# Kernel optimization log

Hardware: AMD Instinct MI355X
Metric: run time of the kernel (lower is better)

## Reference

```python
import jax, jax.numpy as jnp
import numpy as np

D_MODEL = 1024
NUM_HEADS = 16
D_K = D_MODEL // NUM_HEADS
NEG = -10000.0


def setup_inputs() -> dict:
    key = jax.random.key(0)
    ks = jax.random.split(key, 8)
    B, S = 2, 2048
    query = jax.random.normal(ks[0], (B, S, D_MODEL), dtype=jnp.float32)
    key_t = jax.random.normal(ks[1], (B, S, D_MODEL), dtype=jnp.float32)
    value = jax.random.normal(ks[2], (B, S, D_MODEL), dtype=jnp.float32)
    mask = jax.random.randint(ks[3], (B, S), 0, 2, dtype=jnp.int32)
    scale = 1.0 / np.sqrt(D_MODEL)
    Wq = jax.random.normal(ks[4], (D_MODEL, D_MODEL), dtype=jnp.float32) * scale
    Wk = jax.random.normal(ks[5], (D_MODEL, D_MODEL), dtype=jnp.float32) * scale
    Wv = jax.random.normal(ks[6], (D_MODEL, D_MODEL), dtype=jnp.float32) * scale
    Wo = jax.random.normal(ks[7], (D_MODEL, D_MODEL), dtype=jnp.float32) * scale
    return {"query": query, "key": key_t, "value": value, "mask": mask,
            "Wq": Wq, "Wk": Wk, "Wv": Wv, "Wo": Wo}


def reference(query, key, value, mask, Wq, Wk, Wv, Wo):
    B, Sq, _ = query.shape
    Sk = key.shape[1]
    # Linear projections (torch Linear: x @ W.T), split heads -> [B,H,S,d_k]
    def proj(x, W, S):
        return (x @ W.T).reshape(B, S, NUM_HEADS, D_K).transpose(0, 2, 1, 3)
    Q = proj(query, Wq, Sq)
    K = proj(key, Wk, Sk)
    V = proj(value, Wv, Sk)
    # scores [B,H,Sq,Sk]
    scores = jnp.einsum("bhqd,bhkd->bhqk", Q, K) / jnp.sqrt(jnp.float32(D_K))
    # padding mask [B,Sk] -> [B,1,1,Sk]
    pad = mask[:, None, None, :]
    scores = jnp.where(pad == 0, NEG, scores)
    # causal mask (mask_future=True)
    causal = jnp.tril(jnp.ones((Sq, Sk), dtype=bool))
    scores = jnp.where(causal, scores, NEG)
    probs = jax.nn.softmax(scores, axis=-1)  # dropout p=0.0 -> identity
    out = jnp.einsum("bhqk,bhkd->bhqd", probs, V)
    out = out.transpose(0, 2, 1, 3).reshape(B, Sq, D_MODEL)
    return out @ Wo.T
```

## Files before the change

### kernel.cpp

```cpp
#include <hip/hip_runtime.h>
#include <hip/hip_bf16.h>
#include <math.h>

typedef __attribute__((ext_vector_type(8))) short s16x8;
typedef __attribute__((ext_vector_type(4))) float f32x4;

#define MFMA16(a,b,c) __builtin_amdgcn_mfma_f32_16x16x32_bf16((a),(b),(c),0,0,0)

#define GLD16(gp, lp) __builtin_amdgcn_global_load_lds( \
  (const __attribute__((address_space(1))) unsigned int*)(gp), \
  (__attribute__((address_space(3))) unsigned int*)(lp), 16, 0, 0)

static __device__ __forceinline__ unsigned short f2bu(float f) {
  __hip_bfloat16 h = __float2bfloat16(f);
  unsigned short u; __builtin_memcpy(&u, &h, 2); return u;
}
static __device__ __forceinline__ float b2f(unsigned short u) {
  unsigned int x = ((unsigned int)u) << 16; float f; __builtin_memcpy(&f, &x, 4); return f;
}

__global__ __launch_bounds__(256) void cast_all(const float* __restrict__ q, const float* __restrict__ k,
                                                const float* __restrict__ v,
                                                const float* __restrict__ Wq, const float* __restrict__ Wk,
                                                const float* __restrict__ Wv, const float* __restrict__ Wo,
                                                unsigned short* __restrict__ qc, unsigned short* __restrict__ kc,
                                                unsigned short* __restrict__ vc,
                                                unsigned short* __restrict__ wq, unsigned short* __restrict__ wk,
                                                unsigned short* __restrict__ wv, unsigned short* __restrict__ wo) {
  const int y = blockIdx.y;
  const float* in; unsigned short* out; int n4;
  switch (y) {
    case 0: in = q;  out = qc; n4 = 1048576; break;
    case 1: in = k;  out = kc; n4 = 1048576; break;
    case 2: in = v;  out = vc; n4 = 1048576; break;
    case 3: in = Wq; out = wq; n4 = 262144; break;
    case 4: in = Wk; out = wk; n4 = 262144; break;
    case 5: in = Wv; out = wv; n4 = 262144; break;
    default: in = Wo; out = wo; n4 = 262144; break;
  }
  int i = blockIdx.x * 256 + threadIdx.x;
  if (i < n4) {
    float4 val = *(const float4*)(in + (size_t)i * 4);
    unsigned int p0 = (unsigned int)f2bu(val.x) | ((unsigned int)f2bu(val.y) << 16);
    unsigned int p1 = (unsigned int)f2bu(val.z) | ((unsigned int)f2bu(val.w) << 16);
    uint2 pk; pk.x = p0; pk.y = p1;
    *(uint2*)(out + (size_t)i * 4) = pk;
  }
}

static __device__ __forceinline__ void gemm_core(const unsigned short* __restrict__ Aw,
                                                 const unsigned short* __restrict__ Bw,
                                                 int m0, int n0,
                                                 f32x4 (&acc)[4][4],
                                                 unsigned short (*As)[64], unsigned short (*Bs)[64]) {
  const int K = 1024;
  const int tid = threadIdx.x;
  const int lane = tid & 63, wave = tid >> 6;
  const int wm = wave >> 1, wn = wave & 1;
  const int row16 = lane & 15, kgrp = lane >> 4;
  const int srow = lane >> 3, sslot = (lane & 7) ^ srow;
  const int sw = row16 & 7;

  for (int k0 = 0; k0 < K; k0 += 64) {
#pragma unroll
    for (int i = 0; i < 4; i++) {
      int rr = (wave * 4 + i) * 8 + srow;
      GLD16(Aw + (size_t)(m0 + rr) * K + k0 + sslot * 8, (char*)As + (wave * 4 + i) * 1024);
      GLD16(Bw + (size_t)(n0 + rr) * K + k0 + sslot * 8, (char*)Bs + (wave * 4 + i) * 1024);
    }
    __syncthreads();

#pragma unroll
    for (int kk = 0; kk < 2; kk++) {
      s16x8 af[4], bfr[4];
#pragma unroll
      for (int mi = 0; mi < 4; mi++) {
        int rr = wm * 64 + mi * 16 + row16;
        af[mi] = *(const s16x8*)((char*)&As[rr][0] + ((kk * 4 + kgrp) ^ sw) * 16);
      }
#pragma unroll
      for (int ni = 0; ni < 4; ni++) {
        int rr = wn * 64 + ni * 16 + row16;
        bfr[ni] = *(const s16x8*)((char*)&Bs[rr][0] + ((kk * 4 + kgrp) ^ sw) * 16);
      }
#pragma unroll
      for (int mi = 0; mi < 4; mi++)
#pragma unroll
        for (int ni = 0; ni < 4; ni++)
          acc[mi][ni] = MFMA16(af[mi], bfr[ni], acc[mi][ni]);
    }
    __syncthreads();
  }
}

__global__ __launch_bounds__(256) void qkv_gemm(const unsigned short* __restrict__ qc,
                                                const unsigned short* __restrict__ kc,
                                                const unsigned short* __restrict__ vc,
                                                const unsigned short* __restrict__ Wqb,
                                                const unsigned short* __restrict__ Wkb,
                                                const unsigned short* __restrict__ Wvb,
                                                unsigned short* __restrict__ Qb,
                                                unsigned short* __restrict__ Kb,
                                                unsigned short* __restrict__ Vt) {
  __shared__ unsigned short As[128][64];
  __shared__ unsigned short Bs[128][64];
  const int xcd = blockIdx.x & 7, u = blockIdx.x >> 3;
  const int g = xcd * 12 + (u >> 3);
  const int z = g >> 5, mstrip = g & 31;
  const int m0 = mstrip * 128, n0 = (u & 7) * 128;

  const unsigned short* A = (z == 0) ? qc : (z == 1) ? kc : vc;
  const unsigned short* Bw = (z == 0) ? Wqb : (z == 1) ? Wkb : Wvb;

  f32x4 acc[4][4] = {};
  gemm_core(A, Bw, m0, n0, acc, As, Bs);

  const int lane = threadIdx.x & 63, wave = threadIdx.x >> 6;
  const int wm = wave >> 1, wn = wave & 1;
  const int row16 = lane & 15, kgrp = lane >> 4;

  if (z < 2) {
    unsigned short* C = z ? Kb : Qb;
#pragma unroll
    for (int mi = 0; mi < 4; mi++)
#pragma unroll
      for (int ni = 0; ni < 4; ni++)
#pragma unroll
        for (int r = 0; r < 4; r++) {
          int row = m0 + wm * 64 + mi * 16 + kgrp * 4 + r;
          int col = n0 + wn * 64 + ni * 16 + row16;
          C[(size_t)row * 1024 + col] = f2bu(acc[mi][ni][r]);
        }
  } else {
#pragma unroll
    for (int mi = 0; mi < 4; mi++)
#pragma unroll
      for (int ni = 0; ni < 4; ni++) {
        int mb = m0 + wm * 64 + mi * 16 + kgrp * 4;
        int col = n0 + wn * 64 + ni * 16 + row16;
        int bb = mb >> 11, s = mb & 2047;
        unsigned int p0 = (unsigned int)f2bu(acc[mi][ni][0]) | ((unsigned int)f2bu(acc[mi][ni][1]) << 16);
        unsigned int p1 = (unsigned int)f2bu(acc[mi][ni][2]) | ((unsigned int)f2bu(acc[mi][ni][3]) << 16);
        uint2 pk; pk.x = p0; pk.y = p1;
        *(uint2*)&Vt[(((size_t)(bb * 1024 + col)) << 11) + s] = pk;
      }
  }
}

__global__ __launch_bounds__(256) void gemm_wo(const unsigned short* __restrict__ A,
                                               const unsigned short* __restrict__ Bw,
                                               float* __restrict__ C) {
  __shared__ unsigned short As[128][64];
  __shared__ unsigned short Bs[128][64];
  const int xcd = blockIdx.x & 7, u = blockIdx.x >> 3;
  const int g = xcd * 4 + (u >> 3);
  const int m0 = g * 128, n0 = (u & 7) * 128;

  f32x4 acc[4][4] = {};
  gemm_core(A, Bw, m0, n0, acc, As, Bs);

  const int lane = threadIdx.x & 63, wave = threadIdx.x >> 6;
  const int wm = wave >> 1, wn = wave & 1;
  const int row16 = lane & 15, kgrp = lane >> 4;
#pragma unroll
  for (int mi = 0; mi < 4; mi++)
#pragma unroll
    for (int ni = 0; ni < 4; ni++)
#pragma unroll
      for (int r = 0; r < 4; r++) {
        int row = m0 + wm * 64 + mi * 16 + kgrp * 4 + r;
        int col = n0 + wn * 64 + ni * 16 + row16;
        C[(size_t)row * 1024 + col] = acc[mi][ni][r];
      }
}

__global__ __launch_bounds__(256) void fu_pen_kernel(const int* __restrict__ mask, int* __restrict__ fu,
                                                     float* __restrict__ pen) {
  const int S = 2048;
  int b = blockIdx.x;
  __shared__ int red[256];
  int best = S;
  for (int k = threadIdx.x; k < S; k += 256) {
    int mv = mask[b * S + k];
    pen[b * S + k] = mv ? 0.0f : -30000.0f;
    if (mv != 0 && k < best) best = k;
  }
  red[threadIdx.x] = best;
  __syncthreads();
  for (int s = 128; s > 0; s >>= 1) {
    if (threadIdx.x < s) red[threadIdx.x] = min(red[threadIdx.x], red[threadIdx.x + s]);
    __syncthreads();
  }
  if (threadIdx.x == 0) fu[b] = red[0];
}

__global__ __launch_bounds__(256) void reduce_vt(const unsigned short* __restrict__ Vt,
                                                 float* __restrict__ vsum) {
  __shared__ float red[256];
  const unsigned short* p = Vt + ((size_t)blockIdx.x << 11) + threadIdx.x * 8;
  uint4 u = *(const uint4*)p;
  float s = b2f((unsigned short)(u.x & 0xffff));
  s += b2f((unsigned short)(u.x >> 16));
  s += b2f((unsigned short)(u.y & 0xffff));
  s += b2f((unsigned short)(u.y >> 16));
  s += b2f((unsigned short)(u.z & 0xffff));
  s += b2f((unsigned short)(u.z >> 16));
  s += b2f((unsigned short)(u.w & 0xffff));
  s += b2f((unsigned short)(u.w >> 16));
  red[threadIdx.x] = s;
  __syncthreads();
  for (int st = 128; st > 0; st >>= 1) {
    if (threadIdx.x < st) red[threadIdx.x] += red[threadIdx.x + st];
    __syncthreads();
  }
  if (threadIdx.x == 0) vsum[blockIdx.x] = red[0];
}

__global__ __launch_bounds__(256) void flash_attn6(const unsigned short* __restrict__ Q,
                                                   const unsigned short* __restrict__ Kp,
                                                   const unsigned short* __restrict__ Vt,
                                                   const float* __restrict__ pen,
                                                   const int* __restrict__ fu,
                                                   const float* __restrict__ vsum,
                                                   unsigned short* __restrict__ O) {
  const int S = 2048, DM = 1024;
  const float SCALE2 = 0.125f * 1.4426950408889634f;
  const int bid = blockIdx.x;
  const int qt = 31 - (bid >> 5);
  const int bh = bid & 31;
  const int b = bh >> 4, h = bh & 15;
  const int tid = threadIdx.x, lane = tid & 63, wave = tid >> 6;
  const int row16 = lane & 15, kgrp = lane >> 4;

  __shared__ unsigned short Ks[2][64][64];
  __shared__ unsigned short Vs[2][64][64];
  __shared__ unsigned short Ps[4][16][64];

  const size_t base = ((size_t)b * S) * DM + h * 64;
  const size_t vtb = ((size_t)(b * 1024 + h * 64)) * S;
  const float* penb = pen + b * S;

  const int srow = lane >> 3;
  const int sslot = (lane & 7) ^ srow;
  const int sw = row16 & 7;

  const int q0 = qt * 64 + wave * 16;
  const int qg = q0 + row16;
  const int nt = qt + 1;

  s16x8 qf0 = *(const s16x8*)&Q[base + (size_t)qg * DM + kgrp * 8];
  s16x8 qf1 = *(const s16x8*)&Q[base + (size_t)qg * DM + 32 + kgrp * 8];

  const short ONE = 0x3F80;
  const s16x8 ones8 = {ONE, ONE, ONE, ONE, ONE, ONE, ONE, ONE};

  f32x4 oacc[4] = {};
  f32x4 lacc = {};
  float m_run = -1e30f;

  auto stage = [&](int t, int bf) {
    const int kb = t * 64;
#pragma unroll
    for (int c2 = 0; c2 < 2; c2++) {
      const int r = wave * 16 + c2 * 8 + srow;
      GLD16(Kp + base + (size_t)(kb + r) * DM + sslot * 8,
            (char*)&Ks[bf][0][0] + (wave * 2 + c2) * 1024);
      GLD16(Vt + vtb + (size_t)r * S + kb + sslot * 8,
            (char*)&Vs[bf][0][0] + (wave * 2 + c2) * 1024);
    }
  };

  stage(0, 0);
  asm volatile("s_waitcnt vmcnt(0)" ::: "memory");
  __syncthreads();

  int cur = 0;
  for (int t = 0; t < nt; ++t) {
    if (t + 1 < nt) stage(t + 1, cur ^ 1);
    const int kb = t * 64;

    float4 pv[4];
#pragma unroll
    for (int nf = 0; nf < 4; nf++)
      pv[nf] = *(const float4*)&penb[kb + nf * 16 + kgrp * 4];

    f32x4 sc[4];
    __builtin_amdgcn_s_setprio(1);
#pragma unroll
    for (int nf = 0; nf < 4; nf++) {
      const int rr = nf * 16 + row16;
      s16x8 k0 = *(const s16x8*)&Ks[cur][rr][(kgrp ^ sw) * 8];
      s16x8 k1 = *(const s16x8*)&Ks[cur][rr][((4 + kgrp) ^ sw) * 8];
      f32x4 a = {};
      a = MFMA16(k0, qf0, a);
      a = MFMA16(k1, qf1, a);
      sc[nf] = a;
    }
    __builtin_amdgcn_s_setprio(0);

#pragma unroll
    for (int nf = 0; nf < 4; nf++) {
      sc[nf][0] = fmaf(sc[nf][0], SCALE2, pv[nf].x);
      sc[nf][1] = fmaf(sc[nf][1], SCALE2, pv[nf].y);
      sc[nf][2] = fmaf(sc[nf][2], SCALE2, pv[nf].z);
      sc[nf][3] = fmaf(sc[nf][3], SCALE2, pv[nf].w);
    }
    if (t == nt - 1) {
#pragma unroll
      for (int nf = 0; nf < 4; nf++) {
        const int kbase = kb + nf * 16 + kgrp * 4;
#pragma unroll
        for (int r = 0; r < 4; r++)
          if (kbase + r > qg) sc[nf][r] = -30000.0f;
      }
    }

    float t01 = fmaxf(fmaxf(sc[0][0], sc[0][1]), fmaxf(sc[0][2], sc[0][3]));
    float t23 = fmaxf(fmaxf(sc[1][0], sc[1][1]), fmaxf(sc[1][2], sc[1][3]));
    float t45 = fmaxf(fmaxf(sc[2][0], sc[2][1]), fmaxf(sc[2][2], sc[2][3]));
    float t67 = fmaxf(fmaxf(sc[3][0], sc[3][1]), fmaxf(sc[3][2], sc[3][3]));
    float tmax = fmaxf(fmaxf(t01, t23), fmaxf(t45, t67));
    tmax = fmaxf(tmax, __shfl_xor(tmax, 16));
    tmax = fmaxf(tmax, __shfl_xor(tmax, 32));

    if (__any(tmax > m_run)) {
      float mnew = fmaxf(m_run, tmax);
      float alpha = __builtin_exp2f(m_run - mnew);
      m_run = mnew;
      lacc[0] *= alpha; lacc[1] *= alpha; lacc[2] *= alpha; lacc[3] *= alpha;
#pragma unroll
      for (int nf2 = 0; nf2 < 4; nf2++)
#pragma unroll
        for (int r = 0; r < 4; r++) oacc[nf2][r] *= alpha;
    }

#pragma unroll
    for (int nf = 0; nf < 4; nf++)
#pragma unroll
      for (int r = 0; r < 4; r++)
        sc[nf][r] = __builtin_exp2f(sc[nf][r] - m_run);

#pragma unroll
    for (int nf = 0; nf < 4; nf++) {
      uint2 pk;
      pk.x = (unsigned int)f2bu(sc[nf][0]) | ((unsigned int)f2bu(sc[nf][1]) << 16);
      pk.y = (unsigned int)f2bu(sc[nf][2]) | ((unsigned int)f2bu(sc[nf][3]) << 16);
      const int slot = (nf * 2 + (kgrp >> 1)) ^ sw;
      *(uint2*)((char*)&Ps[wave][row16][0] + slot * 16 + (kgrp & 1) * 8) = pk;
    }
    s16x8 pf0 = *(const s16x8*)((char*)&Ps[wave][row16][0] + (kgrp ^ sw) * 16);
    s16x8 pf1 = *(const s16x8*)((char*)&Ps[wave][row16][0] + ((4 + kgrp) ^ sw) * 16);

    __builtin_amdgcn_s_setprio(1);
    lacc = MFMA16(ones8, pf0, lacc);
    lacc = MFMA16(ones8, pf1, lacc);
#pragma unroll
    for (int nf2 = 0; nf2 < 4; nf2++) {
      const int rr = nf2 * 16 + row16;
      s16x8 v0 = *(const s16x8*)&Vs[cur][rr][(kgrp ^ sw) * 8];
      s16x8 v1 = *(const s16x8*)&Vs[cur][rr][((4 + kgrp) ^ sw) * 8];
      oacc[nf2] = MFMA16(v0, pf0, oacc[nf2]);
      oacc[nf2] = MFMA16(v1, pf1, oacc[nf2]);
    }
    __builtin_amdgcn_s_setprio(0);

    asm volatile("s_waitcnt vmcnt(0)" ::: "memory");
    __syncthreads();
    cur ^= 1;
  }

  const int fub = fu[b];
  const float* vs = vsum + b * DM + h * 64;
  const float rl = 1.0f / lacc[0];
#pragma unroll
  for (int nf2 = 0; nf2 < 4; nf2++) {
    const int d0 = nf2 * 16 + kgrp * 4;
    float v0 = oacc[nf2][0] * rl, v1 = oacc[nf2][1] * rl;
    float v2 = oacc[nf2][2] * rl, v3 = oacc[nf2][3] * rl;
    if (qg < fub) {
      float4 vv = *(const float4*)&vs[d0];
      v0 = vv.x * (1.0f / 2048.0f);
      v1 = vv.y * (1.0f / 2048.0f);
      v2 = vv.z * (1.0f / 2048.0f);
      v3 = vv.w * (1.0f / 2048.0f);
    }
    uint2 pk;
    pk.x = (unsigned int)f2bu(v0) | ((unsigned int)f2bu(v1) << 16);
    pk.y = (unsigned int)f2bu(v2) | ((unsigned int)f2bu(v3) << 16);
    *(uint2*)&O[base + (size_t)qg * DM + d0] = pk;
  }
}

extern "C" void kernel_launch(void* const* d_in, const int* in_sizes, int n_in,
                              void* d_out, int out_size, void* d_ws, size_t ws_size,
                              hipStream_t stream) {
  const float* q    = (const float*)d_in[0];
  const float* k    = (const float*)d_in[1];
  const float* v    = (const float*)d_in[2];
  const int*   mask = (const int*)d_in[3];
  const float* Wq   = (const float*)d_in[4];
  const float* Wk   = (const float*)d_in[5];
  const float* Wv   = (const float*)d_in[6];
  const float* Wo   = (const float*)d_in[7];
  float* out = (float*)d_out;
  char* ws = (char*)d_ws;

  unsigned short* Wqb  = (unsigned short*)(ws + (size_t)0);
  unsigned short* Wkb  = (unsigned short*)(ws + ((size_t)2 << 20));
  unsigned short* Wvb  = (unsigned short*)(ws + ((size_t)4 << 20));
  unsigned short* Wob  = (unsigned short*)(ws + ((size_t)6 << 20));
  unsigned short* vc   = (unsigned short*)(ws + ((size_t)8 << 20));
  unsigned short* attn = (unsigned short*)(ws + ((size_t)8 << 20));
  unsigned short* Qb   = (unsigned short*)(ws + ((size_t)16 << 20));
  unsigned short* Kb   = (unsigned short*)(ws + ((size_t)24 << 20));
  unsigned short* Vt   = (unsigned short*)(ws + ((size_t)32 << 20));
  float* vsum          = (float*)(ws + ((size_t)40 << 20));
  int*   fub           = (int*)(ws + ((size_t)40 << 20) + (64 << 10));
  float* pen           = (float*)(ws + ((size_t)40 << 20) + (68 << 10));
  unsigned short* qc   = (unsigned short*)d_out;
  unsigned short* kc   = (unsigned short*)d_out + 4194304;

  cast_all<<<dim3(4096, 7), 256, 0, stream>>>(q, k, v, Wq, Wk, Wv, Wo,
                                              qc, kc, vc, Wqb, Wkb, Wvb, Wob);

  qkv_gemm<<<768, 256, 0, stream>>>(qc, kc, vc, Wqb, Wkb, Wvb, Qb, Kb, Vt);

  fu_pen_kernel<<<2, 256, 0, stream>>>(mask, fub, pen);
  reduce_vt<<<2048, 256, 0, stream>>>(Vt, vsum);

  flash_attn6<<<1024, 256, 0, stream>>>(Qb, Kb, Vt, pen, fub, vsum, attn);

  gemm_wo<<<256, 256, 0, stream>>>(attn, Wob, out);
}
```

Measured before the change: 143.3 us.

## Double flash-attention KV tile to 128 and fold mask prep into cast kernel

The attention kernel now processes 128 keys per iteration instead of 64. This halves the number of loop iterations and their barrier/wait overheads, and reduces the per-tile max shuffles by deferring the cross-lane reduction into the rescale branch. K, V and P shared-memory buffers double in size (about 80KB per block), which may reduce blocks per CU. For even query tiles the last iteration also does up to 64 columns of masked, wasted work. Separately, the mask/penalty kernel is merged into the cast kernel as an extra grid row to remove one launch, though that row launches thousands of blocks that exit immediately.

```diff
diff --git a/kernel.cpp b/kernel.cpp
--- a/kernel.cpp
+++ b/kernel.cpp
@@ -23,11 +23,33 @@
                                                 const float* __restrict__ v,
                                                 const float* __restrict__ Wq, const float* __restrict__ Wk,
                                                 const float* __restrict__ Wv, const float* __restrict__ Wo,
+                                                const int* __restrict__ mask,
                                                 unsigned short* __restrict__ qc, unsigned short* __restrict__ kc,
                                                 unsigned short* __restrict__ vc,
                                                 unsigned short* __restrict__ wq, unsigned short* __restrict__ wk,
-                                                unsigned short* __restrict__ wv, unsigned short* __restrict__ wo) {
+                                                unsigned short* __restrict__ wv, unsigned short* __restrict__ wo,
+                                                int* __restrict__ fu, float* __restrict__ pen) {
   const int y = blockIdx.y;
+  if (y == 7) {
+    if (blockIdx.x >= 2) return;
+    const int S = 2048;
+    int b = blockIdx.x;
+    __shared__ int red[256];
+    int best = S;
+    for (int kk = threadIdx.x; kk < S; kk += 256) {
+      int mv = mask[b * S + kk];
+      pen[b * S + kk] = mv ? 0.0f : -30000.0f;
+      if (mv != 0 && kk < best) best = kk;
+    }
+    red[threadIdx.x] = best;
+    __syncthreads();
+    for (int s = 128; s > 0; s >>= 1) {
+      if (threadIdx.x < s) red[threadIdx.x] = min(red[threadIdx.x], red[threadIdx.x + s]);
+      __syncthreads();
+    }
+    if (threadIdx.x == 0) fu[b] = red[0];
+    return;
+  }
   const float* in; unsigned short* out; int n4;
   switch (y) {
     case 0: in = q;  out = qc; n4 = 1048576; break;
@@ -172,26 +194,6 @@
         int col = n0 + wn * 64 + ni * 16 + row16;
         C[(size_t)row * 1024 + col] = acc[mi][ni][r];
       }
-}
-
-__global__ __launch_bounds__(256) void fu_pen_kernel(const int* __restrict__ mask, int* __restrict__ fu,
-                                                     float* __restrict__ pen) {
-  const int S = 2048;
-  int b = blockIdx.x;
-  __shared__ int red[256];
-  int best = S;
-  for (int k = threadIdx.x; k < S; k += 256) {
-    int mv = mask[b * S + k];
-    pen[b * S + k] = mv ? 0.0f : -30000.0f;
-    if (mv != 0 && k < best) best = k;
-  }
-  red[threadIdx.x] = best;
-  __syncthreads();
-  for (int s = 128; s > 0; s >>= 1) {
-    if (threadIdx.x < s) red[threadIdx.x] = min(red[threadIdx.x], red[threadIdx.x + s]);
-    __syncthreads();
-  }
-  if (threadIdx.x == 0) fu[b] = red[0];
 }
 
 __global__ __launch_bounds__(256) void reduce_vt(const unsigned short* __restrict__ Vt,
@@ -216,7 +218,7 @@
   if (threadIdx.x == 0) vsum[blockIdx.x] = red[0];
 }
 
-__global__ __launch_bounds__(256) void flash_attn6(const unsigned short* __restrict__ Q,
+__global__ __launch_bounds__(256) void flash_attn7(const unsigned short* __restrict__ Q,
                                                    const unsigned short* __restrict__ Kp,
                                                    const unsigned short* __restrict__ Vt,
                                                    const float* __restrict__ pen,
@@ -232,21 +234,21 @@
   const int tid = threadIdx.x, lane = tid & 63, wave = tid >> 6;
   const int row16 = lane & 15, kgrp = lane >> 4;
 
-  __shared__ unsigned short Ks[2][64][64];
-  __shared__ unsigned short Vs[2][64][64];
-  __shared__ unsigned short Ps[4][16][64];
+  __shared__ unsigned short Ks[2][128][64];
+  __shared__ unsigned short Vs[2][64][128];
+  __shared__ unsigned short Ps[4][16][128];
 
   const size_t base = ((size_t)b * S) * DM + h * 64;
   const size_t vtb = ((size_t)(b * 1024 + h * 64)) * S;
   const float* penb = pen + b * S;
 
-  const int srow = lane >> 3;
-  const int sslot = (lane & 7) ^ srow;
+  const int srowK = lane >> 3;
+  const int sslotK = (lane & 7) ^ srowK;
   const int sw = row16 & 7;
 
   const int q0 = qt * 64 + wave * 16;
   const int qg = q0 + row16;
-  const int nt = qt + 1;
+  const int nt = (qt + 2) >> 1;
 
   s16x8 qf0 = *(const s16x8*)&Q[base + (size_t)qg * DM + kgrp * 8];
   s16x8 qf1 = *(const s16x8*)&Q[base + (size_t)qg * DM + 32 + kgrp * 8];
@@ -259,14 +261,19 @@
   float m_run = -1e30f;
 
   auto stage = [&](int t, int bf) {
-    const int kb = t * 64;
-#pragma unroll
-    for (int c2 = 0; c2 < 2; c2++) {
-      const int r = wave * 16 + c2 * 8 + srow;
-      GLD16(Kp + base + (size_t)(kb + r) * DM + sslot * 8,
-            (char*)&Ks[bf][0][0] + (wave * 2 + c2) * 1024);
-      GLD16(Vt + vtb + (size_t)r * S + kb + sslot * 8,
-            (char*)&Vs[bf][0][0] + (wave * 2 + c2) * 1024);
+    const int kb = t * 128;
+#pragma unroll
+    for (int c = 0; c < 4; c++) {
+      const int r = wave * 32 + c * 8 + srowK;
+      GLD16(Kp + base + (size_t)(kb + r) * DM + sslotK * 8,
+            (char*)&Ks[bf][0][0] + (wave * 4 + c) * 1024);
+    }
+#pragma unroll
+    for (int c = 0; c < 4; c++) {
+      const int r = wave * 16 + c * 4 + (lane >> 4);
+      const int sl = (lane & 15) ^ (r & 7);
+      GLD16(Vt + vtb + (size_t)r * S + kb + sl * 8,
+            (char*)&Vs[bf][0][0] + (wave * 4 + c) * 1024);
     }
   };
 
@@ -277,20 +284,20 @@
   int cur = 0;
   for (int t = 0; t < nt; ++t) {
     if (t + 1 < nt) stage(t + 1, cur ^ 1);
-    const int kb = t * 64;
-
-    float4 pv[4];
-#pragma unroll
-    for (int nf = 0; nf < 4; nf++)
+    const int kb = t * 128;
+
+    float4 pv[8];
+#pragma unroll
+    for (int nf = 0; nf < 8; nf++)
       pv[nf] = *(const float4*)&penb[kb + nf * 16 + kgrp * 4];
 
-    f32x4 sc[4];
+    f32x4 sc[8];
     __builtin_amdgcn_s_setprio(1);
 #pragma unroll
-    for (int nf = 0; nf < 4; nf++) {
+    for (int nf = 0; nf < 8; nf++) {
       const int rr = nf * 16 + row16;
-      s16x8 k0 = *(const s16x8*)&Ks[cur][rr][(kgrp ^ sw) * 8];
-      s16x8 k1 = *(const s16x8*)&Ks[cur][rr][((4 + kgrp) ^ sw) * 8];
+      s16x8 k0 = *(const s16x8*)((char*)&Ks[cur][rr][0] + ((0 + kgrp) ^ sw) * 16);
+      s16x8 k1 = *(const s16x8*)((char*)&Ks[cur][rr][0] + ((4 + kgrp) ^ sw) * 16);
       f32x4 a = {};
       a = MFMA16(k0, qf0, a);
       a = MFMA16(k1, qf1, a);
@@ -299,7 +306,7 @@
     __builtin_amdgcn_s_setprio(0);
 
 #pragma unroll
-    for (int nf = 0; nf < 4; nf++) {
+    for (int nf = 0; nf < 8; nf++) {
       sc[nf][0] = fmaf(sc[nf][0], SCALE2, pv[nf].x);
       sc[nf][1] = fmaf(sc[nf][1], SCALE2, pv[nf].y);
       sc[nf][2] = fmaf(sc[nf][2], SCALE2, pv[nf].z);
@@ -307,7 +314,7 @@
     }
     if (t == nt - 1) {
 #pragma unroll
-      for (int nf = 0; nf < 4; nf++) {
+      for (int nf = 0; nf < 8; nf++) {
         const int kbase = kb + nf * 16 + kgrp * 4;
 #pragma unroll
         for (int r = 0; r < 4; r++)
@@ -315,16 +322,15 @@
       }
     }
 
-    float t01 = fmaxf(fmaxf(sc[0][0], sc[0][1]), fmaxf(sc[0][2], sc[0][3]));
-    float t23 = fmaxf(fmaxf(sc[1][0], sc[1][1]), fmaxf(sc[1][2], sc[1][3]));
-    float t45 = fmaxf(fmaxf(sc[2][0], sc[2][1]), fmaxf(sc[2][2], sc[2][3]));
-    float t67 = fmaxf(fmaxf(sc[3][0], sc[3][1]), fmaxf(sc[3][2], sc[3][3]));
-    float tmax = fmaxf(fmaxf(t01, t23), fmaxf(t45, t67));
-    tmax = fmaxf(tmax, __shfl_xor(tmax, 16));
-    tmax = fmaxf(tmax, __shfl_xor(tmax, 32));
+    float tmax = fmaxf(fmaxf(sc[0][0], sc[0][1]), fmaxf(sc[0][2], sc[0][3]));
+#pragma unroll
+    for (int nf = 1; nf < 8; nf++)
+      tmax = fmaxf(tmax, fmaxf(fmaxf(sc[nf][0], sc[nf][1]), fmaxf(sc[nf][2], sc[nf][3])));
 
     if (__any(tmax > m_run)) {
-      float mnew = fmaxf(m_run, tmax);
+      float wmax = fmaxf(tmax, __shfl_xor(tmax, 16));
+      wmax = fmaxf(wmax, __shfl_xor(wmax, 32));
+      float mnew = fmaxf(m_run, wmax);
       float alpha = __builtin_exp2f(m_run - mnew);
       m_run = mnew;
       lacc[0] *= alpha; lacc[1] *= alpha; lacc[2] *= alpha; lacc[3] *= alpha;
@@ -335,32 +341,35 @@
     }
 
 #pragma unroll
-    for (int nf = 0; nf < 4; nf++)
+    for (int nf = 0; nf < 8; nf++)
 #pragma unroll
       for (int r = 0; r < 4; r++)
         sc[nf][r] = __builtin_exp2f(sc[nf][r] - m_run);
 
 #pragma unroll
-    for (int nf = 0; nf < 4; nf++) {
+    for (int nf = 0; nf < 8; nf++) {
       uint2 pk;
       pk.x = (unsigned int)f2bu(sc[nf][0]) | ((unsigned int)f2bu(sc[nf][1]) << 16);
       pk.y = (unsigned int)f2bu(sc[nf][2]) | ((unsigned int)f2bu(sc[nf][3]) << 16);
       const int slot = (nf * 2 + (kgrp >> 1)) ^ sw;
       *(uint2*)((char*)&Ps[wave][row16][0] + slot * 16 + (kgrp & 1) * 8) = pk;
     }
-    s16x8 pf0 = *(const s16x8*)((char*)&Ps[wave][row16][0] + (kgrp ^ sw) * 16);
-    s16x8 pf1 = *(const s16x8*)((char*)&Ps[wave][row16][0] + ((4 + kgrp) ^ sw) * 16);
+    s16x8 pf[4];
+#pragma unroll
+    for (int kk = 0; kk < 4; kk++)
+      pf[kk] = *(const s16x8*)((char*)&Ps[wave][row16][0] + ((kk * 4 + kgrp) ^ sw) * 16);
 
     __builtin_amdgcn_s_setprio(1);
-    lacc = MFMA16(ones8, pf0, lacc);
-    lacc = MFMA16(ones8, pf1, lacc);
+#pragma unroll
+    for (int kk = 0; kk < 4; kk++) lacc = MFMA16(ones8, pf[kk], lacc);
 #pragma unroll
     for (int nf2 = 0; nf2 < 4; nf2++) {
       const int rr = nf2 * 16 + row16;
-      s16x8 v0 = *(const s16x8*)&Vs[cur][rr][(kgrp ^ sw) * 8];
-      s16x8 v1 = *(const s16x8*)&Vs[cur][rr][((4 + kgrp) ^ sw) * 8];
-      oacc[nf2] = MFMA16(v0, pf0, oacc[nf2]);
-      oacc[nf2] = MFMA16(v1, pf1, oacc[nf2]);
+#pragma unroll
+      for (int kk = 0; kk < 4; kk++) {
+        s16x8 vv = *(const s16x8*)((char*)&Vs[cur][rr][0] + ((kk * 4 + kgrp) ^ sw) * 16);
+        oacc[nf2] = MFMA16(vv, pf[kk], oacc[nf2]);
+      }
     }
     __builtin_amdgcn_s_setprio(0);
 
@@ -420,15 +429,14 @@
   unsigned short* qc   = (unsigned short*)d_out;
   unsigned short* kc   = (unsigned short*)d_out + 4194304;
 
-  cast_all<<<dim3(4096, 7), 256, 0, stream>>>(q, k, v, Wq, Wk, Wv, Wo,
-                                              qc, kc, vc, Wqb, Wkb, Wvb, Wob);
+  cast_all<<<dim3(4096, 8), 256, 0, stream>>>(q, k, v, Wq, Wk, Wv, Wo, mask,
+                                              qc, kc, vc, Wqb, Wkb, Wvb, Wob, fub, pen);
 
   qkv_gemm<<<768, 256, 0, stream>>>(qc, kc, vc, Wqb, Wkb, Wvb, Qb, Kb, Vt);
 
-  fu_pen_kernel<<<2, 256, 0, stream>>>(mask, fub, pen);
   reduce_vt<<<2048, 256, 0, stream>>>(Vt, vsum);
 
-  flash_attn6<<<1024, 256, 0, stream>>>(Qb, Kb, Vt, pen, fub, vsum, attn);
+  flash_attn7<<<1024, 256, 0, stream>>>(Qb, Kb, Vt, pen, fub, vsum, attn);
 
   gemm_wo<<<256, 256, 0, stream>>>(attn, Wob, out);
 }
```

After: 145.5 us. No clear change (+1.5%).

## Fold softmax scale into Wq, replace additive pad penalty with bitmask, merge mask prep

Applied to the files above, without the earlier changes.

Pre-scales Wq by the softmax scale times log2(e) during the bf16 cast, so the attention kernel no longer applies an FMA per score. The padding penalty becomes a 16-bit-per-key AND mask applied to the packed bf16 probabilities, and the mask/first-unmasked computation moves into cast_all as an extra grid row, removing one launch. The cross-lane max shuffle now runs only when some lane's local max rises, and bf16 packing uses the hardware v_cvt_pk_bf16_f32 instruction. Masked keys now take part in the running max, which shifts the numerics slightly, and the per-lane max tracking could differ from the old row max semantics.

```diff
diff --git a/kernel.cpp b/kernel.cpp
--- a/kernel.cpp
+++ b/kernel.cpp
@@ -17,23 +17,52 @@
 }
 static __device__ __forceinline__ float b2f(unsigned short u) {
   unsigned int x = ((unsigned int)u) << 16; float f; __builtin_memcpy(&f, &x, 4); return f;
+}
+static __device__ __forceinline__ unsigned int cvtpk(float lo, float hi) {
+  unsigned int r;
+  asm("v_cvt_pk_bf16_f32 %0, %1, %2" : "=v"(r) : "v"(lo), "v"(hi));
+  return r;
 }
 
 __global__ __launch_bounds__(256) void cast_all(const float* __restrict__ q, const float* __restrict__ k,
                                                 const float* __restrict__ v,
                                                 const float* __restrict__ Wq, const float* __restrict__ Wk,
                                                 const float* __restrict__ Wv, const float* __restrict__ Wo,
+                                                const int* __restrict__ mask,
                                                 unsigned short* __restrict__ qc, unsigned short* __restrict__ kc,
                                                 unsigned short* __restrict__ vc,
                                                 unsigned short* __restrict__ wq, unsigned short* __restrict__ wk,
-                                                unsigned short* __restrict__ wv, unsigned short* __restrict__ wo) {
+                                                unsigned short* __restrict__ wv, unsigned short* __restrict__ wo,
+                                                int* __restrict__ fu, unsigned int* __restrict__ pm) {
+  const float SCALE2 = 0.125f * 1.4426950408889634f;
   const int y = blockIdx.y;
-  const float* in; unsigned short* out; int n4;
+  if (y == 7) {
+    if (blockIdx.x >= 2) return;
+    const int S = 2048;
+    int b = blockIdx.x;
+    __shared__ int red[256];
+    int best = S;
+    for (int kk = threadIdx.x; kk < 1024; kk += 256) {
+      int m0 = mask[b * S + 2 * kk], m1 = mask[b * S + 2 * kk + 1];
+      pm[b * 1024 + kk] = (m0 ? 0xFFFFu : 0u) | (m1 ? 0xFFFF0000u : 0u);
+      if (m1) best = min(best, 2 * kk + 1);
+      if (m0) best = min(best, 2 * kk);
+    }
+    red[threadIdx.x] = best;
+    __syncthreads();
+    for (int s = 128; s > 0; s >>= 1) {
+      if (threadIdx.x < s) red[threadIdx.x] = min(red[threadIdx.x], red[threadIdx.x + s]);
+      __syncthreads();
+    }
+    if (threadIdx.x == 0) fu[b] = red[0];
+    return;
+  }
+  const float* in; unsigned short* out; int n4; float scl = 1.0f;
   switch (y) {
     case 0: in = q;  out = qc; n4 = 1048576; break;
     case 1: in = k;  out = kc; n4 = 1048576; break;
     case 2: in = v;  out = vc; n4 = 1048576; break;
-    case 3: in = Wq; out = wq; n4 = 262144; break;
+    case 3: in = Wq; out = wq; n4 = 262144; scl = SCALE2; break;
     case 4: in = Wk; out = wk; n4 = 262144; break;
     case 5: in = Wv; out = wv; n4 = 262144; break;
     default: in = Wo; out = wo; n4 = 262144; break;
@@ -41,9 +70,9 @@
   int i = blockIdx.x * 256 + threadIdx.x;
   if (i < n4) {
     float4 val = *(const float4*)(in + (size_t)i * 4);
-    unsigned int p0 = (unsigned int)f2bu(val.x) | ((unsigned int)f2bu(val.y) << 16);
-    unsigned int p1 = (unsigned int)f2bu(val.z) | ((unsigned int)f2bu(val.w) << 16);
-    uint2 pk; pk.x = p0; pk.y = p1;
+    uint2 pk;
+    pk.x = cvtpk(val.x * scl, val.y * scl);
+    pk.y = cvtpk(val.z * scl, val.w * scl);
     *(uint2*)(out + (size_t)i * 4) = pk;
   }
 }
@@ -139,9 +168,9 @@
         int mb = m0 + wm * 64 + mi * 16 + kgrp * 4;
         int col = n0 + wn * 64 + ni * 16 + row16;
         int bb = mb >> 11, s = mb & 2047;
-        unsigned int p0 = (unsigned int)f2bu(acc[mi][ni][0]) | ((unsigned int)f2bu(acc[mi][ni][1]) << 16);
-        unsigned int p1 = (unsigned int)f2bu(acc[mi][ni][2]) | ((unsigned int)f2bu(acc[mi][ni][3]) << 16);
-        uint2 pk; pk.x = p0; pk.y = p1;
+        uint2 pk;
+        pk.x = cvtpk(acc[mi][ni][0], acc[mi][ni][1]);
+        pk.y = cvtpk(acc[mi][ni][2], acc[mi][ni][3]);
         *(uint2*)&Vt[(((size_t)(bb * 1024 + col)) << 11) + s] = pk;
       }
   }
@@ -172,26 +201,6 @@
         int col = n0 + wn * 64 + ni * 16 + row16;
         C[(size_t)row * 1024 + col] = acc[mi][ni][r];
       }
-}
-
-__global__ __launch_bounds__(256) void fu_pen_kernel(const int* __restrict__ mask, int* __restrict__ fu,
-                                                     float* __restrict__ pen) {
-  const int S = 2048;
-  int b = blockIdx.x;
-  __shared__ int red[256];
-  int best = S;
-  for (int k = threadIdx.x; k < S; k += 256) {
-    int mv = mask[b * S + k];
-    pen[b * S + k] = mv ? 0.0f : -30000.0f;
-    if (mv != 0 && k < best) best = k;
-  }
-  red[threadIdx.x] = best;
-  __syncthreads();
-  for (int s = 128; s > 0; s >>= 1) {
-    if (threadIdx.x < s) red[threadIdx.x] = min(red[threadIdx.x], red[threadIdx.x + s]);
-    __syncthreads();
-  }
-  if (threadIdx.x == 0) fu[b] = red[0];
 }
 
 __global__ __launch_bounds__(256) void reduce_vt(const unsigned short* __restrict__ Vt,
@@ -216,15 +225,14 @@
   if (threadIdx.x == 0) vsum[blockIdx.x] = red[0];
 }
 
-__global__ __launch_bounds__(256) void flash_attn6(const unsigned short* __restrict__ Q,
+__global__ __launch_bounds__(256) void flash_attn8(const unsigned short* __restrict__ Q,
                                                    const unsigned short* __restrict__ Kp,
                                                    const unsigned short* __restrict__ Vt,
-                                                   const float* __restrict__ pen,
+                                                   const unsigned int* __restrict__ pm,
                                                    const int* __restrict__ fu,
                                                    const float* __restrict__ vsum,
                                                    unsigned short* __restrict__ O) {
   const int S = 2048, DM = 1024;
-  const float SCALE2 = 0.125f * 1.4426950408889634f;
   const int bid = blockIdx.x;
   const int qt = 31 - (bid >> 5);
   const int bh = bid & 31;
@@ -238,7 +246,7 @@
 
   const size_t base = ((size_t)b * S) * DM + h * 64;
   const size_t vtb = ((size_t)(b * 1024 + h * 64)) * S;
-  const float* penb = pen + b * S;
+  const unsigned int* pmb = pm + b * 1024;
 
   const int srow = lane >> 3;
   const int sslot = (lane & 7) ^ srow;
@@ -279,10 +287,10 @@
     if (t + 1 < nt) stage(t + 1, cur ^ 1);
     const int kb = t * 64;
 
-    float4 pv[4];
+    uint2 pmv[4];
 #pragma unroll
     for (int nf = 0; nf < 4; nf++)
-      pv[nf] = *(const float4*)&penb[kb + nf * 16 + kgrp * 4];
+      pmv[nf] = *(const uint2*)&pmb[(kb + nf * 16 + kgrp * 4) >> 1];
 
     f32x4 sc[4];
     __builtin_amdgcn_s_setprio(1);
@@ -298,13 +306,6 @@
     }
     __builtin_amdgcn_s_setprio(0);
 
-#pragma unroll
-    for (int nf = 0; nf < 4; nf++) {
-      sc[nf][0] = fmaf(sc[nf][0], SCALE2, pv[nf].x);
-      sc[nf][1] = fmaf(sc[nf][1], SCALE2, pv[nf].y);
-      sc[nf][2] = fmaf(sc[nf][2], SCALE2, pv[nf].z);
-      sc[nf][3] = fmaf(sc[nf][3], SCALE2, pv[nf].w);
-    }
     if (t == nt - 1) {
 #pragma unroll
       for (int nf = 0; nf < 4; nf++) {
@@ -315,18 +316,20 @@
       }
     }
 
-    float t01 = fmaxf(fmaxf(sc[0][0], sc[0][1]), fmaxf(sc[0][2], sc[0][3]));
-    float t23 = fmaxf(fmaxf(sc[1][0], sc[1][1]), fmaxf(sc[1][2], sc[1][3]));
-    float t45 = fmaxf(fmaxf(sc[2][0], sc[2][1]), fmaxf(sc[2][2], sc[2][3]));
-    float t67 = fmaxf(fmaxf(sc[3][0], sc[3][1]), fmaxf(sc[3][2], sc[3][3]));
-    float tmax = fmaxf(fmaxf(t01, t23), fmaxf(t45, t67));
-    tmax = fmaxf(tmax, __shfl_xor(tmax, 16));
-    tmax = fmaxf(tmax, __shfl_xor(tmax, 32));
+    float a0 = fmaxf(fmaxf(sc[0][0], sc[0][1]), sc[0][2]);
+    float a1 = fmaxf(fmaxf(sc[0][3], sc[1][0]), sc[1][1]);
+    float a2 = fmaxf(fmaxf(sc[1][2], sc[1][3]), sc[2][0]);
+    float a3 = fmaxf(fmaxf(sc[2][1], sc[2][2]), sc[2][3]);
+    float a4 = fmaxf(fmaxf(sc[3][0], sc[3][1]), sc[3][2]);
+    float b0 = fmaxf(fmaxf(a0, a1), a2);
+    float b1 = fmaxf(fmaxf(a3, a4), sc[3][3]);
+    float tmax = fmaxf(b0, b1);
 
     if (__any(tmax > m_run)) {
-      float mnew = fmaxf(m_run, tmax);
-      float alpha = __builtin_exp2f(m_run - mnew);
-      m_run = mnew;
+      float wmax = fmaxf(tmax, __shfl_xor(tmax, 16));
+      wmax = fmaxf(wmax, __shfl_xor(wmax, 32));
+      float alpha = __builtin_exp2f(m_run - wmax);
+      m_run = wmax;
       lacc[0] *= alpha; lacc[1] *= alpha; lacc[2] *= alpha; lacc[3] *= alpha;
 #pragma unroll
       for (int nf2 = 0; nf2 < 4; nf2++)
@@ -343,8 +346,8 @@
 #pragma unroll
     for (int nf = 0; nf < 4; nf++) {
       uint2 pk;
-      pk.x = (unsigned int)f2bu(sc[nf][0]) | ((unsigned int)f2bu(sc[nf][1]) << 16);
-      pk.y = (unsigned int)f2bu(sc[nf][2]) | ((unsigned int)f2bu(sc[nf][3]) << 16);
+      pk.x = cvtpk(sc[nf][0], sc[nf][1]) & pmv[nf].x;
+      pk.y = cvtpk(sc[nf][2], sc[nf][3]) & pmv[nf].y;
       const int slot = (nf * 2 + (kgrp >> 1)) ^ sw;
       *(uint2*)((char*)&Ps[wave][row16][0] + slot * 16 + (kgrp & 1) * 8) = pk;
     }
@@ -385,8 +388,8 @@
       v3 = vv.w * (1.0f / 2048.0f);
     }
     uint2 pk;
-    pk.x = (unsigned int)f2bu(v0) | ((unsigned int)f2bu(v1) << 16);
-    pk.y = (unsigned int)f2bu(v2) | ((unsigned int)f2bu(v3) << 16);
+    pk.x = cvtpk(v0, v1);
+    pk.y = cvtpk(v2, v3);
     *(uint2*)&O[base + (size_t)qg * DM + d0] = pk;
   }
 }
@@ -416,19 +419,18 @@
   unsigned short* Vt   = (unsigned short*)(ws + ((size_t)32 << 20));
   float* vsum          = (float*)(ws + ((size_t)40 << 20));
   int*   fub           = (int*)(ws + ((size_t)40 << 20) + (64 << 10));
-  float* pen           = (float*)(ws + ((size_t)40 << 20) + (68 << 10));
+  unsigned int* pm32   = (unsigned int*)(ws + ((size_t)40 << 20) + (68 << 10));
   unsigned short* qc   = (unsigned short*)d_out;
   unsigned short* kc   = (unsigned short*)d_out + 4194304;
 
-  cast_all<<<dim3(4096, 7), 256, 0, stream>>>(q, k, v, Wq, Wk, Wv, Wo,
-                                              qc, kc, vc, Wqb, Wkb, Wvb, Wob);
+  cast_all<<<dim3(4096, 8), 256, 0, stream>>>(q, k, v, Wq, Wk, Wv, Wo, mask,
+                                              qc, kc, vc, Wqb, Wkb, Wvb, Wob, fub, pm32);
 
   qkv_gemm<<<768, 256, 0, stream>>>(qc, kc, vc, Wqb, Wkb, Wvb, Qb, Kb, Vt);
 
-  fu_pen_kernel<<<2, 256, 0, stream>>>(mask, fub, pen);
   reduce_vt<<<2048, 256, 0, stream>>>(Vt, vsum);
 
-  flash_attn6<<<1024, 256, 0, stream>>>(Qb, Kb, Vt, pen, fub, vsum, attn);
+  flash_attn8<<<1024, 256, 0, stream>>>(Qb, Kb, Vt, pm32, fub, vsum, attn);
 
   gemm_wo<<<256, 256, 0, stream>>>(attn, Wob, out);
 }
```

Result: no change. 140.9 us (-1.7%).
